# Kernel optimization log

Measured on AMD Instinct MI355X. Metric: run time of the kernel, lower is better.

## Reference

```python
import jax, jax.numpy as jnp
import numpy as np

N_NODES = 100000
N_EDGES = 3200000
IN_DIM = 512
HID_DIM = 16
OUT_DIM = 64


def _gcn_layer(E, X, W, b, n_nodes):
    # Standard GCN layer (CatGNN GCNLayer_MPNN_2):
    # add self-loops, symmetric deg^-1/2 normalization, project, gather-scatter sum.
    src = jnp.concatenate([E[0], jnp.arange(n_nodes, dtype=E.dtype)])
    dst = jnp.concatenate([E[1], jnp.arange(n_nodes, dtype=E.dtype)])
    deg = jax.ops.segment_sum(jnp.ones_like(dst, dtype=X.dtype), dst, num_segments=n_nodes)
    dinv = jnp.where(deg > 0, jax.lax.rsqrt(deg), 0.0)  # deg^-1/2, safe
    h = X @ W  # [N, d_out] project BEFORE aggregation (cheaper gather)
    norm = dinv[src] * dinv[dst]  # [E+N]
    msg = h[src] * norm[:, None]  # gather + scale
    out = jax.ops.segment_sum(msg, dst, num_segments=n_nodes)  # scatter-sum
    return out + b


def setup_inputs() -> dict:
    key = jax.random.key(0)
    k1, k2, k3, k4, k5 = jax.random.split(key, 5)
    V = jnp.arange(N_NODES, dtype=jnp.int64)
    E = jax.random.randint(k1, (2, N_EDGES), 0, N_NODES, dtype=jnp.int64)
    X = jax.random.normal(k2, (N_NODES, IN_DIM), dtype=jnp.float32)
    # Glorot-style init for layer weights
    W1 = jax.random.normal(k3, (IN_DIM, HID_DIM), dtype=jnp.float32) / np.sqrt(IN_DIM)
    b1 = jnp.zeros((HID_DIM,), dtype=jnp.float32)
    W2 = jax.random.normal(k4, (HID_DIM, OUT_DIM), dtype=jnp.float32) / np.sqrt(HID_DIM)
    b2 = jnp.zeros((OUT_DIM,), dtype=jnp.float32)
    return {"V": V, "E": E, "X": X, "W1": W1, "b1": b1, "W2": W2, "b2": b2}


def reference(V, E, X, W1, b1, W2, b2):
    n_nodes = V.shape[0]
    H = jax.nn.relu(_gcn_layer(E, X, W1, b1, n_nodes))
    # dropout is identity in eval mode
    H = _gcn_layer(E, H, W2, b2, n_nodes)
    return H
```

## Files before the change

kernel.cpp:

```cpp
#include <hip/hip_runtime.h>

#define HID 16
#define ODIM 64
#define IDIM 512
#define BKB 8
#define BKS 256
#define PTILE 8192
#define PITER 16
#define PAD 16

__device__ __forceinline__ int wave_scan_block(int v, int t, int* wsum) {
    int lane = t & 63, w = t >> 6;
    int x = v;
#pragma unroll
    for (int off = 1; off < 64; off <<= 1) {
        int y = __shfl_up(x, off, 64);
        if (lane >= off) x += y;
    }
    if (lane == 63) wsum[w] = x;
    __syncthreads();
    if (w == 0) {
        int s = (lane < 8) ? wsum[lane] : 0;
#pragma unroll
        for (int off = 1; off < 8; off <<= 1) {
            int y = __shfl_up(s, off, 64);
            if (lane >= off) s += y;
        }
        if (lane < 8) wsum[lane] = s;
    }
    __syncthreads();
    return x + (w ? wsum[w - 1] : 0);
}

__global__ __launch_bounds__(512) void k_bhist(const int* __restrict__ dst,
                                               int* __restrict__ bcnt, int ne, int nbk) {
    __shared__ int h[512];
    int t = threadIdx.x;
    h[t] = 0;
    __syncthreads();
    int stride = gridDim.x * 512;
    for (int e = blockIdx.x * 512 + t; e < ne; e += stride)
        atomicAdd(&h[dst[e] >> BKB], 1);
    __syncthreads();
    if (t < nbk && h[t]) atomicAdd(&bcnt[t * PAD], h[t]);
}

__global__ __launch_bounds__(512) void k_bscan(const int* __restrict__ bcnt,
                                               int* __restrict__ bbase,
                                               int* __restrict__ bcur, int nbk) {
    __shared__ int wsum[8];
    int t = threadIdx.x;
    int v = (t < nbk) ? bcnt[t * PAD] : 0;
    int inc = wave_scan_block(v, t, wsum);
    if (t < nbk) { int b = inc - v; bbase[t] = b; bcur[t * PAD] = b; }
}

__global__ __launch_bounds__(512) void k_part(const int* __restrict__ src,
                                              const int* __restrict__ dst,
                                              int* __restrict__ bcur,
                                              unsigned int* __restrict__ ebuf, int ne) {
    __shared__ int h[512], sc[512], base[512], lcur[512], wsum[8];
    __shared__ unsigned int sval[PTILE];
    __shared__ int saddr[PTILE];
    int e0 = blockIdx.x * PTILE;
    int m = ne - e0; if (m > PTILE) m = PTILE;
    int t = threadIdx.x;
    h[t] = 0;
    __syncthreads();
    int dv[PITER];
#pragma unroll
    for (int it = 0; it < PITER; ++it) {
        int k = t + it * 512;
        int d = 0;
        if (k < m) { d = dst[e0 + k]; atomicAdd(&h[d >> BKB], 1); }
        dv[it] = d;
    }
    __syncthreads();
    int hv = h[t];
    int inc = wave_scan_block(hv, t, wsum);
    sc[t] = inc;
    base[t] = hv ? atomicAdd(&bcur[t * PAD], hv) : 0;
    lcur[t] = 0;
    __syncthreads();
#pragma unroll
    for (int it = 0; it < PITER; ++it) {
        int k = t + it * 512;
        if (k < m) {
            int d = dv[it];
            int b = d >> BKB;
            int r = atomicAdd(&lcur[b], 1);
            int slot = sc[b] - h[b] + r;
            sval[slot] = ((unsigned int)src[e0 + k] << BKB) | (unsigned int)(d & (BKS - 1));
            saddr[slot] = base[b] + r;
        }
    }
    __syncthreads();
#pragma unroll
    for (int it = 0; it < PITER; ++it) {
        int k = t + it * 512;
        if (k < m) ebuf[saddr[k]] = sval[k];
    }
}

__global__ __launch_bounds__(512) void k_csr(const int* __restrict__ bbase,
                                             const int* __restrict__ bcnt,
                                             const unsigned int* __restrict__ ebuf,
                                             int* __restrict__ cnt,
                                             int* __restrict__ row_start,
                                             int* __restrict__ csr_src, int n) {
    __shared__ int h[256], sc[256], lc[256], wsum[8];
    int bk = blockIdx.x;
    int node0 = bk << BKB;
    int ebase = bbase[bk];
    int ecnt = bcnt[bk * PAD];
    int t = threadIdx.x;
    if (t < 256) { h[t] = 0; lc[t] = 0; }
    __syncthreads();
    for (int k = t; k < ecnt; k += 512) atomicAdd(&h[ebuf[ebase + k] & (BKS - 1)], 1);
    __syncthreads();
    int hv = (t < 256) ? h[t] : 0;
    int inc = wave_scan_block(hv, t, wsum);
    if (t < 256) {
        sc[t] = inc;
        int node = node0 + t;
        if (node < n) { cnt[node] = hv; row_start[node] = ebase + inc - hv; }
    }
    __syncthreads();
    for (int k = t; k < ecnt; k += 512) {
        unsigned int p = ebuf[ebase + k];
        int dl = p & (BKS - 1);
        int r = atomicAdd(&lc[dl], 1);
        csr_src[ebase + sc[dl] - h[dl] + r] = (int)(p >> BKB);
    }
}

__device__ __forceinline__ void fmaq(float4& a, float s, float4 w) {
    a.x = fmaf(s, w.x, a.x);
    a.y = fmaf(s, w.y, a.y);
    a.z = fmaf(s, w.z, a.z);
    a.w = fmaf(s, w.w, a.w);
}

__global__ __launch_bounds__(256) void k_proj1(const float* __restrict__ X,
                                               const float* __restrict__ W1,
                                               const int* __restrict__ cnt,
                                               float* __restrict__ hs1, int n) {
    int i = blockIdx.x * 256 + threadIdx.x;
    if (i >= n) return;

    const float4* __restrict__ xr = (const float4*)(X + (size_t)i * IDIM);
    const float4* __restrict__ W4 = (const float4*)W1;
    float4 a0 = make_float4(0.f, 0.f, 0.f, 0.f), a1 = a0, a2 = a0, a3 = a0;

#pragma unroll 4
    for (int k4 = 0; k4 < IDIM / 4; ++k4) {
        float4 x = xr[k4];
        const float4* w = W4 + k4 * 16;
        fmaq(a0, x.x, w[0]);  fmaq(a1, x.x, w[1]);  fmaq(a2, x.x, w[2]);  fmaq(a3, x.x, w[3]);
        fmaq(a0, x.y, w[4]);  fmaq(a1, x.y, w[5]);  fmaq(a2, x.y, w[6]);  fmaq(a3, x.y, w[7]);
        fmaq(a0, x.z, w[8]);  fmaq(a1, x.z, w[9]);  fmaq(a2, x.z, w[10]); fmaq(a3, x.z, w[11]);
        fmaq(a0, x.w, w[12]); fmaq(a1, x.w, w[13]); fmaq(a2, x.w, w[14]); fmaq(a3, x.w, w[15]);
    }

    float di = rsqrtf((float)(cnt[i] + 1));
    a0.x *= di; a0.y *= di; a0.z *= di; a0.w *= di;
    a1.x *= di; a1.y *= di; a1.z *= di; a1.w *= di;
    a2.x *= di; a2.y *= di; a2.z *= di; a2.w *= di;
    a3.x *= di; a3.y *= di; a3.z *= di; a3.w *= di;
    float4* h4 = (float4*)(hs1 + (size_t)i * HID);
    h4[0] = a0; h4[1] = a1; h4[2] = a2; h4[3] = a3;
}

__device__ __forceinline__ void acc4(float4& a, float4 v) {
    a.x += v.x; a.y += v.y; a.z += v.z; a.w += v.w;
}

__device__ __forceinline__ float4 gacc(int rs, int c, int q,
                                       const int* __restrict__ csr_src,
                                       const float4* __restrict__ h4,
                                       float4 acc) {
    float4 acc2 = make_float4(0.f, 0.f, 0.f, 0.f);
    int k = 0;
    int head = (-rs) & 3;
    if (head > c) head = c;
    for (; k < head; ++k)
        acc4(acc, h4[(size_t)csr_src[rs + k] * 4 + q]);
    for (; k + 7 < c; k += 8) {
        int4 s0 = *(const int4*)(csr_src + rs + k);
        int4 s1 = *(const int4*)(csr_src + rs + k + 4);
        float4 v0 = h4[(size_t)s0.x * 4 + q];
        float4 v1 = h4[(size_t)s0.y * 4 + q];
        float4 v2 = h4[(size_t)s0.z * 4 + q];
        float4 v3 = h4[(size_t)s0.w * 4 + q];
        float4 w0 = h4[(size_t)s1.x * 4 + q];
        float4 w1 = h4[(size_t)s1.y * 4 + q];
        float4 w2 = h4[(size_t)s1.z * 4 + q];
        float4 w3 = h4[(size_t)s1.w * 4 + q];
        acc4(acc, v0);  acc4(acc2, w0);
        acc4(acc, v1);  acc4(acc2, w1);
        acc4(acc, v2);  acc4(acc2, w2);
        acc4(acc, v3);  acc4(acc2, w3);
    }
    for (; k + 3 < c; k += 4) {
        int4 s = *(const int4*)(csr_src + rs + k);
        acc4(acc, h4[(size_t)s.x * 4 + q]);
        acc4(acc2, h4[(size_t)s.y * 4 + q]);
        acc4(acc, h4[(size_t)s.z * 4 + q]);
        acc4(acc2, h4[(size_t)s.w * 4 + q]);
    }
    for (; k < c; ++k)
        acc4(acc, h4[(size_t)csr_src[rs + k] * 4 + q]);
    acc4(acc, acc2);
    return acc;
}

__global__ __launch_bounds__(256) void k_gather_mid(const int* __restrict__ row_start,
                                                    const int* __restrict__ cnt,
                                                    const int* __restrict__ csr_src,
                                                    const float* __restrict__ hs,
                                                    const float* __restrict__ b1,
                                                    float* __restrict__ outbuf, int n) {
    int tid = blockIdx.x * blockDim.x + threadIdx.x;
    int i = tid >> 2;
    int q = tid & 3;
    if (i >= n) return;
    const float4* h4 = (const float4*)hs;
    int rs = row_start[i];
    int c = cnt[i];
    float4 acc = gacc(rs, c, q, csr_src, h4, h4[(size_t)i * 4 + q]);
    float di = rsqrtf((float)(c + 1));
    float4 b = ((const float4*)b1)[q];
    float4 r;
    r.x = fmaxf(fmaf(di, acc.x, b.x), 0.f) * di;
    r.y = fmaxf(fmaf(di, acc.y, b.y), 0.f) * di;
    r.z = fmaxf(fmaf(di, acc.z, b.z), 0.f) * di;
    r.w = fmaxf(fmaf(di, acc.w, b.w), 0.f) * di;
    ((float4*)outbuf)[(size_t)i * 4 + q] = r;
}

__global__ __launch_bounds__(256) void k_gather(const int* __restrict__ row_start,
                                                const int* __restrict__ cnt,
                                                const int* __restrict__ csr_src,
                                                const float* __restrict__ hs,
                                                float* __restrict__ agg, int n) {
    int tid = blockIdx.x * blockDim.x + threadIdx.x;
    int i = tid >> 2;
    int q = tid & 3;
    if (i >= n) return;
    const float4* h4 = (const float4*)hs;
    int rs = row_start[i];
    int c = cnt[i];
    float4 acc = gacc(rs, c, q, csr_src, h4, h4[(size_t)i * 4 + q]);
    ((float4*)agg)[(size_t)i * 4 + q] = acc;
}

__global__ __launch_bounds__(256) void k_out(const int* __restrict__ cnt,
                                             const float* __restrict__ agg2,
                                             const float* __restrict__ W2,
                                             const float* __restrict__ b2,
                                             float* __restrict__ out, int n) {
    __shared__ float Ws[HID * ODIM];
    __shared__ float bs[ODIM];
    int t = threadIdx.x;
    for (int u = t; u < HID * ODIM; u += 256) Ws[u] = W2[u];
    if (t < ODIM) bs[t] = b2[t];
    __syncthreads();

    int j = t & 63;
    int slot = t >> 6;
    int i0 = blockIdx.x * 16 + slot * 4;

    float wc[HID];
#pragma unroll
    for (int k = 0; k < HID; ++k) wc[k] = Ws[k * ODIM + j];
    float bj = bs[j];

    const float4* g4 = (const float4*)agg2;
#pragma unroll
    for (int u = 0; u < 4; ++u) {
        int i = i0 + u;
        if (i < n) {
            float4 g0 = g4[(size_t)i * 4 + 0];
            float4 g1 = g4[(size_t)i * 4 + 1];
            float4 g2 = g4[(size_t)i * 4 + 2];
            float4 g3 = g4[(size_t)i * 4 + 3];
            float acc = g0.x * wc[0]  + g0.y * wc[1]  + g0.z * wc[2]  + g0.w * wc[3]
                      + g1.x * wc[4]  + g1.y * wc[5]  + g1.z * wc[6]  + g1.w * wc[7]
                      + g2.x * wc[8]  + g2.y * wc[9]  + g2.z * wc[10] + g2.w * wc[11]
                      + g3.x * wc[12] + g3.y * wc[13] + g3.z * wc[14] + g3.w * wc[15];
            float di = rsqrtf((float)(cnt[i] + 1));
            out[(size_t)i * ODIM + j] = fmaf(di, acc, bj);
        }
    }
}

extern "C" void kernel_launch(void* const* d_in, const int* in_sizes, int n_in,
                              void* d_out, int out_size, void* d_ws, size_t ws_size,
                              hipStream_t stream) {
    const int* E = (const int*)d_in[1];
    const float* X = (const float*)d_in[2];
    const float* W1 = (const float*)d_in[3];
    const float* b1 = (const float*)d_in[4];
    const float* W2 = (const float*)d_in[5];
    const float* b2 = (const float*)d_in[6];
    float* out = (float*)d_out;

    const int n = in_sizes[0];
    const int ne = in_sizes[1] / 2;
    const int* src = E;
    const int* dst = E + ne;
    const int nbk = (n + BKS - 1) >> BKB;

    char* ws = (char*)d_ws;
    int* bcnt = (int*)ws;
    int* bbase = (int*)(ws + (32u << 10));
    int* bcur = (int*)(ws + (64u << 10));
    int* cnt = (int*)(ws + (1u << 20));
    int* row_start = (int*)(ws + (2u << 20));
    unsigned int* ebuf = (unsigned int*)(ws + (3u << 20));
    float* B1 = (float*)(ws + (3u << 20));
    float* B2 = (float*)(ws + (10u << 20));
    int* csr_src = (int*)(ws + (17u << 20));

    hipMemsetAsync(bcnt, 0, nbk * PAD * sizeof(int), stream);
    k_bhist<<<256, 512, 0, stream>>>(dst, bcnt, ne, nbk);
    k_bscan<<<1, 512, 0, stream>>>(bcnt, bbase, bcur, nbk);
    k_part<<<(ne + PTILE - 1) / PTILE, 512, 0, stream>>>(src, dst, bcur, ebuf, ne);
    k_csr<<<nbk, 512, 0, stream>>>(bbase, bcnt, ebuf, cnt, row_start, csr_src, n);

    k_proj1<<<(n + 255) / 256, 256, 0, stream>>>(X, W1, cnt, B1, n);
    k_gather_mid<<<(n * 4 + 255) / 256, 256, 0, stream>>>(row_start, cnt, csr_src, B1, b1, B2, n);
    k_gather<<<(n * 4 + 255) / 256, 256, 0, stream>>>(row_start, cnt, csr_src, B2, B1, n);
    k_out<<<(n + 15) / 16, 256, 0, stream>>>(cnt, B1, W2, b2, out, n);
}
```

Before: 498.7 us.

## Replace full CSR build with bucketed edge lists and LDS atomic aggregation

Drops the second-level CSR sort (k_csr) and the LDS staging in the partition kernel. The partition now writes packed edges straight into per-bucket ranges, and a counting kernel only produces in-degrees. Aggregation runs one block per 256-node bucket and accumulates gathered source rows into a padded shared-memory tile with float atomics. The aim is to cut sorting passes and scattered CSR writes, at the cost of uncoalesced partition writes, many LDS float atomics, and only about 391 blocks for the aggregation.

```diff
diff --git a/kernel.cpp b/kernel.cpp
--- a/kernel.cpp
+++ b/kernel.cpp
@@ -8,6 +8,20 @@
 #define PTILE 8192
 #define PITER 16
 #define PAD 16
+#define APAD 17
+
+__global__ __launch_bounds__(512) void k_bhist(const int* __restrict__ dst,
+                                               int* __restrict__ bcnt, int ne, int nbk) {
+    __shared__ int h[512];
+    int t = threadIdx.x;
+    h[t] = 0;
+    __syncthreads();
+    int stride = gridDim.x * 512;
+    for (int e = blockIdx.x * 512 + t; e < ne; e += stride)
+        atomicAdd(&h[dst[e] >> BKB], 1);
+    __syncthreads();
+    if (t < nbk && h[t]) atomicAdd(&bcnt[t * PAD], h[t]);
+}
 
 __device__ __forceinline__ int wave_scan_block(int v, int t, int* wsum) {
     int lane = t & 63, w = t >> 6;
@@ -30,19 +44,6 @@
     }
     __syncthreads();
     return x + (w ? wsum[w - 1] : 0);
-}
-
-__global__ __launch_bounds__(512) void k_bhist(const int* __restrict__ dst,
-                                               int* __restrict__ bcnt, int ne, int nbk) {
-    __shared__ int h[512];
-    int t = threadIdx.x;
-    h[t] = 0;
-    __syncthreads();
-    int stride = gridDim.x * 512;
-    for (int e = blockIdx.x * 512 + t; e < ne; e += stride)
-        atomicAdd(&h[dst[e] >> BKB], 1);
-    __syncthreads();
-    if (t < nbk && h[t]) atomicAdd(&bcnt[t * PAD], h[t]);
 }
 
 __global__ __launch_bounds__(512) void k_bscan(const int* __restrict__ bcnt,
@@ -59,9 +60,7 @@
                                               const int* __restrict__ dst,
                                               int* __restrict__ bcur,
                                               unsigned int* __restrict__ ebuf, int ne) {
-    __shared__ int h[512], sc[512], base[512], lcur[512], wsum[8];
-    __shared__ unsigned int sval[PTILE];
-    __shared__ int saddr[PTILE];
+    __shared__ int h[512], base[512], lcur[512];
     int e0 = blockIdx.x * PTILE;
     int m = ne - e0; if (m > PTILE) m = PTILE;
     int t = threadIdx.x;
@@ -77,8 +76,6 @@
     }
     __syncthreads();
     int hv = h[t];
-    int inc = wave_scan_block(hv, t, wsum);
-    sc[t] = inc;
     base[t] = hv ? atomicAdd(&bcur[t * PAD], hv) : 0;
     lcur[t] = 0;
     __syncthreads();
@@ -89,49 +86,27 @@
             int d = dv[it];
             int b = d >> BKB;
             int r = atomicAdd(&lcur[b], 1);
-            int slot = sc[b] - h[b] + r;
-            sval[slot] = ((unsigned int)src[e0 + k] << BKB) | (unsigned int)(d & (BKS - 1));
-            saddr[slot] = base[b] + r;
-        }
-    }
-    __syncthreads();
-#pragma unroll
-    for (int it = 0; it < PITER; ++it) {
-        int k = t + it * 512;
-        if (k < m) ebuf[saddr[k]] = sval[k];
-    }
-}
-
-__global__ __launch_bounds__(512) void k_csr(const int* __restrict__ bbase,
+            ebuf[base[b] + r] =
+                ((unsigned int)src[e0 + k] << BKB) | (unsigned int)(d & (BKS - 1));
+        }
+    }
+}
+
+__global__ __launch_bounds__(512) void k_cnt(const int* __restrict__ bbase,
                                              const int* __restrict__ bcnt,
                                              const unsigned int* __restrict__ ebuf,
-                                             int* __restrict__ cnt,
-                                             int* __restrict__ row_start,
-                                             int* __restrict__ csr_src, int n) {
-    __shared__ int h[256], sc[256], lc[256], wsum[8];
+                                             int* __restrict__ cnt, int n) {
+    __shared__ int h[256];
     int bk = blockIdx.x;
-    int node0 = bk << BKB;
     int ebase = bbase[bk];
     int ecnt = bcnt[bk * PAD];
     int t = threadIdx.x;
-    if (t < 256) { h[t] = 0; lc[t] = 0; }
+    if (t < 256) h[t] = 0;
     __syncthreads();
     for (int k = t; k < ecnt; k += 512) atomicAdd(&h[ebuf[ebase + k] & (BKS - 1)], 1);
     __syncthreads();
-    int hv = (t < 256) ? h[t] : 0;
-    int inc = wave_scan_block(hv, t, wsum);
-    if (t < 256) {
-        sc[t] = inc;
-        int node = node0 + t;
-        if (node < n) { cnt[node] = hv; row_start[node] = ebase + inc - hv; }
-    }
-    __syncthreads();
-    for (int k = t; k < ecnt; k += 512) {
-        unsigned int p = ebuf[ebase + k];
-        int dl = p & (BKS - 1);
-        int r = atomicAdd(&lc[dl], 1);
-        csr_src[ebase + sc[dl] - h[dl] + r] = (int)(p >> BKB);
-    }
+    int node = (bk << BKB) + t;
+    if (t < 256 && node < n) cnt[node] = h[t];
 }
 
 __device__ __forceinline__ void fmaq(float4& a, float s, float4 w) {
@@ -171,87 +146,71 @@
     h4[0] = a0; h4[1] = a1; h4[2] = a2; h4[3] = a3;
 }
 
-__device__ __forceinline__ void acc4(float4& a, float4 v) {
-    a.x += v.x; a.y += v.y; a.z += v.z; a.w += v.w;
-}
-
-__device__ __forceinline__ float4 gacc(int rs, int c, int q,
-                                       const int* __restrict__ csr_src,
-                                       const float4* __restrict__ h4,
-                                       float4 acc) {
-    float4 acc2 = make_float4(0.f, 0.f, 0.f, 0.f);
-    int k = 0;
-    int head = (-rs) & 3;
-    if (head > c) head = c;
-    for (; k < head; ++k)
-        acc4(acc, h4[(size_t)csr_src[rs + k] * 4 + q]);
-    for (; k + 7 < c; k += 8) {
-        int4 s0 = *(const int4*)(csr_src + rs + k);
-        int4 s1 = *(const int4*)(csr_src + rs + k + 4);
-        float4 v0 = h4[(size_t)s0.x * 4 + q];
-        float4 v1 = h4[(size_t)s0.y * 4 + q];
-        float4 v2 = h4[(size_t)s0.z * 4 + q];
-        float4 v3 = h4[(size_t)s0.w * 4 + q];
-        float4 w0 = h4[(size_t)s1.x * 4 + q];
-        float4 w1 = h4[(size_t)s1.y * 4 + q];
-        float4 w2 = h4[(size_t)s1.z * 4 + q];
-        float4 w3 = h4[(size_t)s1.w * 4 + q];
-        acc4(acc, v0);  acc4(acc2, w0);
-        acc4(acc, v1);  acc4(acc2, w1);
-        acc4(acc, v2);  acc4(acc2, w2);
-        acc4(acc, v3);  acc4(acc2, w3);
-    }
-    for (; k + 3 < c; k += 4) {
-        int4 s = *(const int4*)(csr_src + rs + k);
-        acc4(acc, h4[(size_t)s.x * 4 + q]);
-        acc4(acc2, h4[(size_t)s.y * 4 + q]);
-        acc4(acc, h4[(size_t)s.z * 4 + q]);
-        acc4(acc2, h4[(size_t)s.w * 4 + q]);
-    }
-    for (; k < c; ++k)
-        acc4(acc, h4[(size_t)csr_src[rs + k] * 4 + q]);
-    acc4(acc, acc2);
-    return acc;
-}
-
-__global__ __launch_bounds__(256) void k_gather_mid(const int* __restrict__ row_start,
-                                                    const int* __restrict__ cnt,
-                                                    const int* __restrict__ csr_src,
-                                                    const float* __restrict__ hs,
-                                                    const float* __restrict__ b1,
-                                                    float* __restrict__ outbuf, int n) {
-    int tid = blockIdx.x * blockDim.x + threadIdx.x;
-    int i = tid >> 2;
-    int q = tid & 3;
-    if (i >= n) return;
-    const float4* h4 = (const float4*)hs;
-    int rs = row_start[i];
-    int c = cnt[i];
-    float4 acc = gacc(rs, c, q, csr_src, h4, h4[(size_t)i * 4 + q]);
-    float di = rsqrtf((float)(c + 1));
-    float4 b = ((const float4*)b1)[q];
-    float4 r;
-    r.x = fmaxf(fmaf(di, acc.x, b.x), 0.f) * di;
-    r.y = fmaxf(fmaf(di, acc.y, b.y), 0.f) * di;
-    r.z = fmaxf(fmaf(di, acc.z, b.z), 0.f) * di;
-    r.w = fmaxf(fmaf(di, acc.w, b.w), 0.f) * di;
-    ((float4*)outbuf)[(size_t)i * 4 + q] = r;
-}
-
-__global__ __launch_bounds__(256) void k_gather(const int* __restrict__ row_start,
-                                                const int* __restrict__ cnt,
-                                                const int* __restrict__ csr_src,
-                                                const float* __restrict__ hs,
-                                                float* __restrict__ agg, int n) {
-    int tid = blockIdx.x * blockDim.x + threadIdx.x;
-    int i = tid >> 2;
-    int q = tid & 3;
-    if (i >= n) return;
-    const float4* h4 = (const float4*)hs;
-    int rs = row_start[i];
-    int c = cnt[i];
-    float4 acc = gacc(rs, c, q, csr_src, h4, h4[(size_t)i * 4 + q]);
-    ((float4*)agg)[(size_t)i * 4 + q] = acc;
+template <int MODE>
+__global__ __launch_bounds__(512) void k_agg(const int* __restrict__ bbase,
+                                             const int* __restrict__ bcnt,
+                                             const unsigned int* __restrict__ ebuf,
+                                             const float* __restrict__ hs,
+                                             const int* __restrict__ cnt,
+                                             const float* __restrict__ b1,
+                                             float* __restrict__ outb, int n) {
+    __shared__ float acc[BKS * APAD];
+    int bk = blockIdx.x;
+    int node0 = bk << BKB;
+    int ebase = bbase[bk];
+    int ecnt = bcnt[bk * PAD];
+    int t = threadIdx.x;
+
+    for (int u = t; u < BKS * HID; u += 512) {
+        int dl = u >> 4, j = u & 15;
+        int node = node0 + dl;
+        acc[dl * APAD + j] = (node < n) ? hs[(size_t)node * HID + j] : 0.f;
+    }
+    __syncthreads();
+
+    int k = t;
+    for (; k + 512 < ecnt; k += 1024) {
+        unsigned int p0 = ebuf[ebase + k];
+        unsigned int p1 = ebuf[ebase + k + 512];
+        const float4* r0 = (const float4*)(hs + (size_t)(p0 >> BKB) * HID);
+        const float4* r1 = (const float4*)(hs + (size_t)(p1 >> BKB) * HID);
+        float4 a0 = r0[0], a1 = r0[1], a2 = r0[2], a3 = r0[3];
+        float4 c0 = r1[0], c1 = r1[1], c2 = r1[2], c3 = r1[3];
+        float* d0 = &acc[(int)(p0 & (BKS - 1)) * APAD];
+        float* d1 = &acc[(int)(p1 & (BKS - 1)) * APAD];
+        atomicAdd(&d0[0], a0.x);  atomicAdd(&d0[1], a0.y);  atomicAdd(&d0[2], a0.z);  atomicAdd(&d0[3], a0.w);
+        atomicAdd(&d0[4], a1.x);  atomicAdd(&d0[5], a1.y);  atomicAdd(&d0[6], a1.z);  atomicAdd(&d0[7], a1.w);
+        atomicAdd(&d0[8], a2.x);  atomicAdd(&d0[9], a2.y);  atomicAdd(&d0[10], a2.z); atomicAdd(&d0[11], a2.w);
+        atomicAdd(&d0[12], a3.x); atomicAdd(&d0[13], a3.y); atomicAdd(&d0[14], a3.z); atomicAdd(&d0[15], a3.w);
+        atomicAdd(&d1[0], c0.x);  atomicAdd(&d1[1], c0.y);  atomicAdd(&d1[2], c0.z);  atomicAdd(&d1[3], c0.w);
+        atomicAdd(&d1[4], c1.x);  atomicAdd(&d1[5], c1.y);  atomicAdd(&d1[6], c1.z);  atomicAdd(&d1[7], c1.w);
+        atomicAdd(&d1[8], c2.x);  atomicAdd(&d1[9], c2.y);  atomicAdd(&d1[10], c2.z); atomicAdd(&d1[11], c2.w);
+        atomicAdd(&d1[12], c3.x); atomicAdd(&d1[13], c3.y); atomicAdd(&d1[14], c3.z); atomicAdd(&d1[15], c3.w);
+    }
+    if (k < ecnt) {
+        unsigned int p0 = ebuf[ebase + k];
+        const float4* r0 = (const float4*)(hs + (size_t)(p0 >> BKB) * HID);
+        float4 a0 = r0[0], a1 = r0[1], a2 = r0[2], a3 = r0[3];
+        float* d0 = &acc[(int)(p0 & (BKS - 1)) * APAD];
+        atomicAdd(&d0[0], a0.x);  atomicAdd(&d0[1], a0.y);  atomicAdd(&d0[2], a0.z);  atomicAdd(&d0[3], a0.w);
+        atomicAdd(&d0[4], a1.x);  atomicAdd(&d0[5], a1.y);  atomicAdd(&d0[6], a1.z);  atomicAdd(&d0[7], a1.w);
+        atomicAdd(&d0[8], a2.x);  atomicAdd(&d0[9], a2.y);  atomicAdd(&d0[10], a2.z); atomicAdd(&d0[11], a2.w);
+        atomicAdd(&d0[12], a3.x); atomicAdd(&d0[13], a3.y); atomicAdd(&d0[14], a3.z); atomicAdd(&d0[15], a3.w);
+    }
+    __syncthreads();
+
+    for (int u = t; u < BKS * HID; u += 512) {
+        int dl = u >> 4, j = u & 15;
+        int node = node0 + dl;
+        if (node < n) {
+            float v = acc[dl * APAD + j];
+            if (MODE == 1) {
+                float di = rsqrtf((float)(cnt[node] + 1));
+                v = fmaxf(fmaf(di, v, b1[j]), 0.f) * di;
+            }
+            outb[(size_t)node * HID + j] = v;
+        }
+    }
 }
 
 __global__ __launch_bounds__(256) void k_out(const int* __restrict__ cnt,
@@ -316,20 +275,18 @@
     int* bbase = (int*)(ws + (32u << 10));
     int* bcur = (int*)(ws + (64u << 10));
     int* cnt = (int*)(ws + (1u << 20));
-    int* row_start = (int*)(ws + (2u << 20));
     unsigned int* ebuf = (unsigned int*)(ws + (3u << 20));
-    float* B1 = (float*)(ws + (3u << 20));
-    float* B2 = (float*)(ws + (10u << 20));
-    int* csr_src = (int*)(ws + (17u << 20));
+    float* B1 = (float*)(ws + (17u << 20));
+    float* B2 = (float*)(ws + (24u << 20));
 
     hipMemsetAsync(bcnt, 0, nbk * PAD * sizeof(int), stream);
     k_bhist<<<256, 512, 0, stream>>>(dst, bcnt, ne, nbk);
     k_bscan<<<1, 512, 0, stream>>>(bcnt, bbase, bcur, nbk);
     k_part<<<(ne + PTILE - 1) / PTILE, 512, 0, stream>>>(src, dst, bcur, ebuf, ne);
-    k_csr<<<nbk, 512, 0, stream>>>(bbase, bcnt, ebuf, cnt, row_start, csr_src, n);
+    k_cnt<<<nbk, 512, 0, stream>>>(bbase, bcnt, ebuf, cnt, n);
 
     k_proj1<<<(n + 255) / 256, 256, 0, stream>>>(X, W1, cnt, B1, n);
-    k_gather_mid<<<(n * 4 + 255) / 256, 256, 0, stream>>>(row_start, cnt, csr_src, B1, b1, B2, n);
-    k_gather<<<(n * 4 + 255) / 256, 256, 0, stream>>>(row_start, cnt, csr_src, B2, B1, n);
+    k_agg<1><<<nbk, 512, 0, stream>>>(bbase, bcnt, ebuf, B1, cnt, b1, B2, n);
+    k_agg<0><<<nbk, 512, 0, stream>>>(bbase, bcnt, ebuf, B2, cnt, b1, B1, n);
     k_out<<<(n + 15) / 16, 256, 0, stream>>>(cnt, B1, W2, b2, out, n);
 }
```

New measurement: 1.114 ms. 2.23x slower.
